# Kernel optimization log

Hardware: AMD Instinct MI355X
Metric: run time of the kernel (lower is better)

## Reference

```python
import jax, jax.numpy as jnp
import numpy as np

EPS = 1e-6
NUM_SPECIAL = 4
NUM_HEADS = 16


def _rms_norm(x, w, eps=EPS):
    # x: [..., d], normalize over last dim
    var = jnp.mean(jnp.square(x), axis=-1, keepdims=True)
    return x * jax.lax.rsqrt(var + eps) * w


def _rotate_half(x):
    d = x.shape[-1] // 2
    return jnp.concatenate([-x[..., d:], x[..., :d]], axis=-1)


def _apply_rotary(q, k, cos, sin):
    # q,k: [B,H,N,hd]; cos,sin: [N,hd] -> broadcast [1,1,N,hd]
    cos = cos[None, None, :, :]
    sin = sin[None, None, :, :]
    q_out = q * cos + _rotate_half(q) * sin
    k_out = k * cos + _rotate_half(k) * sin
    return q_out, k_out


def _make_2d_mask(seq_len, num_special, window):
    # special tokens attend / are attended fully; patches use 2D local box
    patch_len = seq_len - num_special
    gs = int(round(patch_len ** 0.5))
    idx = jnp.arange(seq_len)
    special = idx < num_special
    p = idx - num_special
    row = p // gs
    col = p % gs
    special_case = special[:, None] | special[None, :]
    swa = (jnp.abs(row[:, None] - row[None, :]) <= window) & (
        jnp.abs(col[:, None] - col[None, :]) <= window)
    return special_case | swa  # [N, N] bool


def setup_inputs() -> dict:
    key = jax.random.key(0)
    ks = jax.random.split(key, 7)
    B, N, C = 4, 1028, 1024
    hd = C // NUM_HEADS
    return {
        "hidden_states": jax.random.normal(ks[0], (B, N, C), dtype=jnp.float32),
        "cos": jax.random.uniform(ks[1], (N, hd), dtype=jnp.float32),
        "sin": jax.random.uniform(ks[2], (N, hd), dtype=jnp.float32),
        "qkv_w": jax.random.normal(ks[3], (3 * C, C), dtype=jnp.float32) * (C ** -0.5),
        "out_w": jax.random.normal(ks[4], (C, C), dtype=jnp.float32) * (C ** -0.5),
        "norm_q_w": jnp.ones((hd,), dtype=jnp.float32),
        "norm_k_w": jnp.ones((hd,), dtype=jnp.float32),
        "sliding_window": 2,
    }


def reference(hidden_states, cos, sin, qkv_w, out_w, norm_q_w, norm_k_w, sliding_window):
    B, N, C = hidden_states.shape
    H = NUM_HEADS
    hd = C // H

    # fused QKV projection (nn.Linear: x @ W^T)
    qkv = jnp.einsum('bnc,dc->bnd', hidden_states, qkv_w)
    qkv = qkv.reshape(B, N, 3, H, hd).transpose(2, 0, 3, 1, 4)  # [3,B,H,N,hd]
    q, k, v = qkv[0], qkv[1], qkv[2]

    # per-head-dim RMSNorm on q and k
    q = _rms_norm(q, norm_q_w)
    k = _rms_norm(k, norm_k_w)

    # RoPE
    q, k = _apply_rotary(q, k, cos, sin)

    # 2D sliding-window + special-token mask
    mask = _make_2d_mask(N, NUM_SPECIAL, sliding_window)  # [N,N]

    scale = 1.0 / jnp.sqrt(jnp.asarray(hd, dtype=q.dtype))
    scores = jnp.einsum('bhqd,bhkd->bhqk', q, k) * scale
    neg = jnp.asarray(jnp.finfo(scores.dtype).min, dtype=scores.dtype)
    scores = jnp.where(mask[None, None, :, :], scores, neg)
    probs = jax.nn.softmax(scores, axis=-1)
    attn = jnp.einsum('bhqk,bhkd->bhqd', probs, v)  # [B,H,N,hd]

    attn = attn.transpose(0, 2, 1, 3).reshape(B, N, C)
    return jnp.einsum('bnc,dc->bnd', attn, out_w)
```

## Files before the change

kernel.cpp:

```cpp
#include <hip/hip_runtime.h>
#include <hip/hip_bf16.h>
#include <stdint.h>

typedef __bf16 bf16;
typedef __attribute__((ext_vector_type(8))) __bf16 bf16x8;
typedef __attribute__((ext_vector_type(4))) __bf16 bf16x4;
typedef __attribute__((ext_vector_type(4))) float f32x4;

#define NSEQ 1028
#define CDIM 1024
#define NHEADS 16
#define HD 64
#define BHN 64
#define NPAD 1088
#define M_REAL 4112
#define M_PAD 4224
#define M_PAD256 4352

static __device__ __forceinline__ void async_copy16(bf16* lds, const bf16* g) {
  __builtin_amdgcn_global_load_lds(
      (const __attribute__((address_space(1))) uint32_t*)g,
      (__attribute__((address_space(3))) uint32_t*)lds, 16, 0, 0);
}

__global__ __launch_bounds__(256) void cast_pad_kernel(const float* __restrict__ src,
                                                       bf16* __restrict__ dst,
                                                       long n_src, long n_dst) {
  long t = (long)blockIdx.x * 256 + threadIdx.x;
  long stride = (long)gridDim.x * 256;
  for (long j = t * 4; j < n_dst; j += stride * 4) {
    bf16x4 o;
    if (j + 4 <= n_src) {
      float4 v = *(const float4*)(src + j);
      o[0] = (bf16)v.x; o[1] = (bf16)v.y; o[2] = (bf16)v.z; o[3] = (bf16)v.w;
    } else {
      for (int k = 0; k < 4; k++) o[k] = (bf16)((j + k < n_src) ? src[j + k] : 0.0f);
    }
    *(bf16x4*)(dst + j) = o;
  }
}

__global__ __launch_bounds__(512, 2) void gemm_qkv_256(
    const bf16* __restrict__ A, const bf16* __restrict__ Bm,
    bf16* __restrict__ q_bf, bf16* __restrict__ k_bf, bf16* __restrict__ v_raw,
    const float* __restrict__ cosb, const float* __restrict__ sinb,
    const float* __restrict__ nqw, const float* __restrict__ nkw) {
  constexpr int K = CDIM;
  constexpr int NT = K / 64;
  __shared__ __attribute__((aligned(16))) bf16 As[2 * 2 * 128 * 64];
  __shared__ __attribute__((aligned(16))) bf16 Bs[2 * 2 * 128 * 64];
  const int tid = threadIdx.x;
  const int lane = tid & 63;
  const int wid = tid >> 6;
  const int wr = wid >> 2;
  const int wc = wid & 3;
  const int l15 = lane & 15, l4 = lane >> 4;
  const int rsw = l15 & 7;

  const int nwg = gridDim.x;
  const int qq = nwg >> 3, rr = nwg & 7;
  const int xcd = blockIdx.x & 7, pos = blockIdx.x >> 3;
  const int work = (xcd < rr ? xcd * (qq + 1) : rr * (qq + 1) + (xcd - rr) * qq) + pos;
  const int n0 = (work % 12) << 8;
  const int m0 = (work / 12) << 8;

  f32x4 acc[8][4] = {};
  bf16x8 afr[4][2], bfr0[2][2], bfr1[2][2];

  size_t a_src[2], b_src[2];
#pragma unroll
  for (int s = 0; s < 2; s++) {
    int idx = tid + s * 512;
    int row = idx >> 3, ch = idx & 7, chs = ch ^ (row & 7);
    a_src[s] = (size_t)(m0 + row) * K + (chs << 3);
    b_src[s] = (size_t)(n0 + row) * K + (chs << 3);
  }

#define STAGE_A(bufi, h, tt)                                                   \
  { _Pragma("unroll") for (int s = 0; s < 2; s++)                              \
      async_copy16(&As[((bufi) * 2 + (h)) * 8192 + (tid + s * 512) * 8],       \
                   A + a_src[s] + (size_t)(h) * (128 * K) + (size_t)(tt) * 64); }
#define STAGE_B(bufi, h, tt)                                                   \
  { _Pragma("unroll") for (int s = 0; s < 2; s++)                              \
      async_copy16(&Bs[((bufi) * 2 + (h)) * 8192 + (tid + s * 512) * 8],       \
                   Bm + b_src[s] + (size_t)(h) * (128 * K) + (size_t)(tt) * 64); }
#define LDA_FRAG(mq)                                                           \
  { _Pragma("unroll") for (int ii = 0; ii < 4; ii++)                           \
      _Pragma("unroll") for (int kk = 0; kk < 2; kk++)                         \
        afr[ii][kk] = *(const bf16x8*)&As[abase + (((mq)*4 + ii) * 16 + l15) * 64 + \
                                          (((kk * 4 + l4) ^ rsw) << 3)]; }
#define LDB_FRAG(dst, nq)                                                      \
  { _Pragma("unroll") for (int jj = 0; jj < 2; jj++)                           \
      _Pragma("unroll") for (int kk = 0; kk < 2; kk++)                         \
        dst[jj][kk] = *(const bf16x8*)&Bs[bbase + ((wc & 1) * 64 + ((nq)*2 + jj) * 16 + l15) * 64 + \
                                          (((kk * 4 + l4) ^ rsw) << 3)]; }
#define MFMA_Q(mq, nq, bb)                                                     \
  { _Pragma("unroll") for (int ii = 0; ii < 4; ii++)                           \
      _Pragma("unroll") for (int jj = 0; jj < 2; jj++)                         \
        _Pragma("unroll") for (int kk = 0; kk < 2; kk++)                       \
          acc[(mq)*4 + ii][(nq)*2 + jj] = __builtin_amdgcn_mfma_f32_16x16x32_bf16( \
              afr[ii][kk], bb[jj][kk], acc[(mq)*4 + ii][(nq)*2 + jj], 0, 0, 0); }

  STAGE_A(0, 0, 0); STAGE_A(0, 1, 0); STAGE_B(0, 0, 0); STAGE_B(0, 1, 0);
  STAGE_B(1, 0, 1); STAGE_B(1, 1, 1);
  asm volatile("s_waitcnt vmcnt(4)" ::: "memory");
  __builtin_amdgcn_s_barrier();

  for (int t = 0; t < NT; ++t) {
    const int cur = t & 1, nxt = cur ^ 1;
    const int abase = (cur * 2 + wr) * 8192;
    const int bbase = (cur * 2 + (wc >> 1)) * 8192;
    LDA_FRAG(0); LDB_FRAG(bfr0, 0);
    if (t + 1 < NT) STAGE_A(nxt, 0, t + 1);
    __builtin_amdgcn_s_barrier();
    asm volatile("s_waitcnt lgkmcnt(0)" ::: "memory");
    __builtin_amdgcn_sched_barrier(0);
    __builtin_amdgcn_s_setprio(1);
    MFMA_Q(0, 0, bfr0);
    __builtin_amdgcn_s_setprio(0);
    __builtin_amdgcn_s_barrier();
    LDB_FRAG(bfr1, 1);
    if (t + 1 < NT) STAGE_A(nxt, 1, t + 1);
    __builtin_amdgcn_s_barrier();
    asm volatile("s_waitcnt lgkmcnt(0)" ::: "memory");
    __builtin_amdgcn_sched_barrier(0);
    __builtin_amdgcn_s_setprio(1);
    MFMA_Q(0, 1, bfr1);
    __builtin_amdgcn_s_setprio(0);
    __builtin_amdgcn_s_barrier();
    LDA_FRAG(1);
    if (t + 2 < NT) STAGE_B(cur, 0, t + 2);
    __builtin_amdgcn_s_barrier();
    asm volatile("s_waitcnt lgkmcnt(0)" ::: "memory");
    __builtin_amdgcn_sched_barrier(0);
    __builtin_amdgcn_s_setprio(1);
    MFMA_Q(1, 0, bfr0);
    __builtin_amdgcn_s_setprio(0);
    __builtin_amdgcn_s_barrier();
    if (t + 2 < NT) {
      STAGE_B(cur, 1, t + 2);
      asm volatile("s_waitcnt vmcnt(4)" ::: "memory");
    } else {
      asm volatile("s_waitcnt vmcnt(0)" ::: "memory");
    }
    __builtin_amdgcn_s_barrier();
    __builtin_amdgcn_s_setprio(1);
    MFMA_Q(1, 1, bfr1);
    __builtin_amdgcn_s_setprio(0);
    __builtin_amdgcn_s_barrier();
  }
#undef STAGE_A
#undef STAGE_B
#undef LDA_FRAG
#undef LDB_FRAG
#undef MFMA_Q

  const int d_base = n0 + wc * 64;
  const int tsel = d_base >> 10;
  const int hh = (d_base & 1023) >> 6;
  if (tsel == 2) {
#pragma unroll
    for (int i = 0; i < 8; i++)
#pragma unroll
      for (int r = 0; r < 4; r++) {
        int m = m0 + wr * 128 + i * 16 + l4 * 4 + r;
        if (m < M_REAL) {
          int b = m / NSEQ, n = m % NSEQ;
          size_t rb = ((size_t)(b * NHEADS + hh) * NSEQ + n) * HD;
#pragma unroll
          for (int j = 0; j < 4; j++)
            v_raw[rb + j * 16 + l15] = (bf16)acc[i][j][r];
        }
      }
  } else {
    const float* wn = (tsel == 0) ? nqw : nkw;
    bf16* dst = (tsel == 0) ? q_bf : k_bf;
    float wv[4];
#pragma unroll
    for (int j = 0; j < 4; j++) wv[j] = wn[j * 16 + l15];
#pragma unroll
    for (int i = 0; i < 8; i++)
#pragma unroll
      for (int r = 0; r < 4; r++) {
        int m = m0 + wr * 128 + i * 16 + l4 * 4 + r;
        if (m >= M_REAL) continue;
        float ss = 0.0f;
#pragma unroll
        for (int j = 0; j < 4; j++) { float x = acc[i][j][r]; ss += x * x; }
        ss += __shfl_xor(ss, 1);
        ss += __shfl_xor(ss, 2);
        ss += __shfl_xor(ss, 4);
        ss += __shfl_xor(ss, 8);
        float rms = rsqrtf(ss * (1.0f / HD) + 1e-6f);
        int b = m / NSEQ, n = m % NSEQ;
        float qn[4];
#pragma unroll
        for (int j = 0; j < 4; j++) qn[j] = acc[i][j][r] * rms * wv[j];
        size_t rb = ((size_t)(b * NHEADS + hh) * NPAD + n) * HD;
#pragma unroll
        for (int j = 0; j < 4; j++) {
          float c = cosb[n * HD + j * 16 + l15];
          float s = sinb[n * HD + j * 16 + l15];
          float rot = (j < 2) ? -qn[j + 2] : qn[j - 2];
          dst[rb + j * 16 + l15] = (bf16)(qn[j] * c + rot * s);
        }
      }
  }
}

__global__ __launch_bounds__(256) void gemm_out_kernel(
    const bf16* __restrict__ A, const bf16* __restrict__ Bm, int K, int N, int Mreal,
    float* __restrict__ outF) {
  __shared__ __attribute__((aligned(16))) bf16 As[2][128 * 64];
  __shared__ __attribute__((aligned(16))) bf16 Bs[2][128 * 64];
  const int tid = threadIdx.x;
  const int lane = tid & 63;
  const int wid = tid >> 6;
  const int wr = wid >> 1, wc = wid & 1;
  const int l15 = lane & 15, l4 = lane >> 4;

  const int nwg = gridDim.x;
  const int cpx = nwg >> 3;
  const int work = (blockIdx.x & 7) * cpx + (blockIdx.x >> 3);
  const int ntx = N >> 7;
  const int n0 = (work % ntx) << 7;
  const int m0 = (work / ntx) << 7;

  f32x4 acc[4][4] = {};

  size_t a_base[4], b_base[4];
#pragma unroll
  for (int s = 0; s < 4; s++) {
    int c = tid + s * 256;
    int row = c >> 3, ch = c & 7;
    int chs = ch ^ (row & 7);
    a_base[s] = (size_t)(m0 + row) * K + (chs << 3);
    b_base[s] = (size_t)(n0 + row) * K + (chs << 3);
  }

#define STAGE(bufi, ktof)                                         \
  {                                                               \
    _Pragma("unroll")                                             \
    for (int s = 0; s < 4; s++) {                                 \
      int c = tid + s * 256;                                      \
      async_copy16(&As[bufi][c * 8], A + a_base[s] + (ktof));     \
      async_copy16(&Bs[bufi][c * 8], Bm + b_base[s] + (ktof));    \
    }                                                             \
  }

  const int nt = K >> 6;
  STAGE(0, 0);

  for (int t = 0; t < nt; ++t) {
    if (t + 1 < nt) {
      STAGE((t + 1) & 1, (t + 1) << 6);
      asm volatile("s_waitcnt vmcnt(8)" ::: "memory");
    } else {
      asm volatile("s_waitcnt vmcnt(0)" ::: "memory");
    }
    __builtin_amdgcn_s_barrier();

    const int rsw = l15 & 7;
    const int cur = t & 1;
    bf16x8 af[2][4], bfr[2][4];
#pragma unroll
    for (int h = 0; h < 2; h++)
#pragma unroll
      for (int i = 0; i < 4; i++)
        af[h][i] = *(const bf16x8*)&As[cur][(wr * 64 + i * 16 + l15) * 64 +
                                            (((h * 4 + l4) ^ rsw) << 3)];
#pragma unroll
    for (int h = 0; h < 2; h++)
#pragma unroll
      for (int j = 0; j < 4; j++)
        bfr[h][j] = *(const bf16x8*)&Bs[cur][(wc * 64 + j * 16 + l15) * 64 +
                                             (((h * 4 + l4) ^ rsw) << 3)];

#pragma unroll
    for (int h = 0; h < 2; h++)
#pragma unroll
      for (int i = 0; i < 4; i++)
#pragma unroll
        for (int j = 0; j < 4; j++)
          acc[i][j] = __builtin_amdgcn_mfma_f32_16x16x32_bf16(af[h][i], bfr[h][j], acc[i][j], 0, 0, 0);

    asm volatile("s_waitcnt lgkmcnt(0)" ::: "memory");
    __builtin_amdgcn_s_barrier();
  }
#undef STAGE

#pragma unroll
  for (int i = 0; i < 4; i++)
#pragma unroll
    for (int j = 0; j < 4; j++) {
      int d = n0 + wc * 64 + j * 16 + l15;
      int mrow = m0 + wr * 64 + i * 16 + l4 * 4;
#pragma unroll
      for (int r = 0; r < 4; r++) {
        int m = mrow + r;
        if (m < Mreal) outF[(size_t)m * N + d] = acc[i][j][r];
      }
    }
}

__global__ __launch_bounds__(256) void v_transpose_kernel(const bf16* __restrict__ v_raw,
                                                          bf16* __restrict__ vT) {
  __shared__ bf16 tile[64][65];
  int bh = blockIdx.y, c = blockIdx.x;
  int tid = threadIdx.x;
#pragma unroll
  for (int jj = 0; jj < 16; jj++) {
    int idx = tid + jj * 256;
    int i = idx >> 6, e = idx & 63;
    int n = (c == 0) ? i : (64 * c - 60 + i);
    bool ok = (c == 0) ? (i < 4) : (n < NSEQ);
    tile[i][e] = ok ? v_raw[((size_t)bh * NSEQ + n) * HD + e] : (bf16)0.0f;
  }
  __syncthreads();
#pragma unroll
  for (int jj = 0; jj < 16; jj++) {
    int idx = tid + jj * 256;
    int e = idx >> 6, i = idx & 63;
    vT[((size_t)bh * HD + e) * NPAD + 64 * c + i] = tile[i][e];
  }
}

__global__ __launch_bounds__(256) void attn_kernel(
    const bf16* __restrict__ Q, const bf16* __restrict__ Kb, const bf16* __restrict__ Vt,
    bf16* __restrict__ att, const int* __restrict__ winp) {
  __shared__ __attribute__((aligned(16))) bf16 P_s[4][16][72];
  __shared__ float o_s[4][4][64];
  __shared__ float ml_s[4][2][16];
  const int bh = blockIdx.y, qt = blockIdx.x;
  const int W = winp[0];
  const int tid = threadIdx.x, w = tid >> 6, lane = tid & 63;
  const int l15 = lane & 15, l4 = lane >> 4;
  const size_t qkbase = (size_t)bh * NPAD * HD;
  const size_t vtb = (size_t)bh * HD * NPAD;
  const bool is_spec = (qt == 16);

  const int qrow0 = is_spec ? 0 : (4 + qt * 64 + w * 16);
  bf16x8 aq0 = *(const bf16x8*)&Q[qkbase + (size_t)(qrow0 + l15) * HD + l4 * 8];
  bf16x8 aq1 = *(const bf16x8*)&Q[qkbase + (size_t)(qrow0 + l15) * HD + 32 + l4 * 8];

  float mrow[4], lrow[4];
  f32x4 o[4] = {};
#pragma unroll
  for (int r = 0; r < 4; r++) { mrow[r] = -1e30f; lrow[r] = 0.0f; }

  int p0, pstep, pmax, toff;
  if (is_spec) {
    p0 = w; pstep = 4; pmax = 16; toff = -1;
  } else {
    int ta = ((2 * qt - W + 64) >> 1) - 32;
    int tb = (2 * qt + 1 + W) >> 1;
    ta = ta < 0 ? 0 : ta;
    tb = tb > 15 ? 15 : tb;
    p0 = 0; pstep = 1; pmax = tb - ta + 1; toff = ta - 1;
  }

  for (int p = p0; p <= pmax; p += pstep) {
    const bool sp = (p == 0);
    const int tau = toff + p;
    const int krow0 = sp ? 0 : (4 + tau * 64);
    const int vcol0 = sp ? 0 : (64 + tau * 64);

    f32x4 sacc[4] = {};
#pragma unroll
    for (int kf = 0; kf < 4; kf++) {
      const bf16* kp = &Kb[qkbase + (size_t)(krow0 + kf * 16 + l15) * HD];
      bf16x8 b0 = *(const bf16x8*)(kp + l4 * 8);
      bf16x8 b1 = *(const bf16x8*)(kp + 32 + l4 * 8);
      sacc[kf] = __builtin_amdgcn_mfma_f32_16x16x32_bf16(aq0, b0, sacc[kf], 0, 0, 0);
      sacc[kf] = __builtin_amdgcn_mfma_f32_16x16x32_bf16(aq1, b1, sacc[kf], 0, 0, 0);
    }

    float pvv[4][4];
#pragma unroll
    for (int kf = 0; kf < 4; kf++)
#pragma unroll
      for (int r = 0; r < 4; r++) {
        float s = sacc[kf][r] * 0.125f;
        bool valid;
        if (sp) {
          valid = (kf == 0) && (l15 < 4);
        } else if (is_spec) {
          valid = true;
        } else {
          int p_k = tau * 64 + kf * 16 + l15;
          int p_q = qt * 64 + w * 16 + l4 * 4 + r;
          int dr = (p_q >> 5) - (p_k >> 5); dr = dr < 0 ? -dr : dr;
          int dc = (p_q & 31) - (p_k & 31); dc = dc < 0 ? -dc : dc;
          valid = (dr <= W) && (dc <= W);
        }
        pvv[kf][r] = valid ? s : -1e30f;
      }

#pragma unroll
    for (int r = 0; r < 4; r++) {
      float mx = fmaxf(fmaxf(pvv[0][r], pvv[1][r]), fmaxf(pvv[2][r], pvv[3][r]));
#pragma unroll
      for (int mm = 1; mm < 16; mm <<= 1) mx = fmaxf(mx, __shfl_xor(mx, mm));
      float mnew = fmaxf(mrow[r], mx);
      float scale = __expf(mrow[r] - mnew);
      float rs = 0.0f;
#pragma unroll
      for (int kf = 0; kf < 4; kf++) {
        float pp = __expf(pvv[kf][r] - mnew);
        pvv[kf][r] = pp;
        rs += pp;
      }
#pragma unroll
      for (int mm = 1; mm < 16; mm <<= 1) rs += __shfl_xor(rs, mm);
      lrow[r] = lrow[r] * scale + rs;
      mrow[r] = mnew;
#pragma unroll
      for (int f = 0; f < 4; f++) o[f][r] *= scale;
    }

#pragma unroll
    for (int kf = 0; kf < 4; kf++)
#pragma unroll
      for (int r = 0; r < 4; r++)
        P_s[w][l4 * 4 + r][kf * 16 + l15] = (bf16)pvv[kf][r];

    bf16x8 pa0 = *(const bf16x8*)&P_s[w][l15][l4 * 8];
    bf16x8 pa1 = *(const bf16x8*)&P_s[w][l15][32 + l4 * 8];
#pragma unroll
    for (int f = 0; f < 4; f++) {
      const bf16* vp = &Vt[vtb + (size_t)(f * 16 + l15) * NPAD + vcol0];
      bf16x8 v0 = *(const bf16x8*)(vp + l4 * 8);
      bf16x8 v1 = *(const bf16x8*)(vp + 32 + l4 * 8);
      o[f] = __builtin_amdgcn_mfma_f32_16x16x32_bf16(pa0, v0, o[f], 0, 0, 0);
      o[f] = __builtin_amdgcn_mfma_f32_16x16x32_bf16(pa1, v1, o[f], 0, 0, 0);
    }
  }

  const int b = bh >> 4, h = bh & 15;
  if (!is_spec) {
#pragma unroll
    for (int f = 0; f < 4; f++)
#pragma unroll
      for (int r = 0; r < 4; r++) {
        int n = qrow0 + l4 * 4 + r;
        att[((size_t)(b * NSEQ + n)) * CDIM + h * HD + f * 16 + l15] =
            (bf16)(o[f][r] / lrow[r]);
      }
  } else {
    if (l4 == 0) {
#pragma unroll
      for (int f = 0; f < 4; f++)
#pragma unroll
        for (int r = 0; r < 4; r++) o_s[w][r][f * 16 + l15] = o[f][r];
      if (l15 == 0)
#pragma unroll
        for (int r = 0; r < 4; r++) { ml_s[w][0][r] = mrow[r]; ml_s[w][1][r] = lrow[r]; }
    }
    __syncthreads();
    int row = tid >> 6, dim = tid & 63;
    float M = -1e30f;
#pragma unroll
    for (int ww = 0; ww < 4; ww++) M = fmaxf(M, ml_s[ww][0][row]);
    float L = 0.0f, val = 0.0f;
#pragma unroll
    for (int ww = 0; ww < 4; ww++) {
      float e = __expf(ml_s[ww][0][row] - M);
      L += e * ml_s[ww][1][row];
      val += e * o_s[ww][row][dim];
    }
    att[((size_t)(b * NSEQ + row)) * CDIM + h * HD + dim] = (bf16)(val / L);
  }
}

extern "C" void kernel_launch(void* const* d_in, const int* in_sizes, int n_in,
                              void* d_out, int out_size, void* d_ws, size_t ws_size,
                              hipStream_t stream) {
  const float* hidden = (const float*)d_in[0];
  const float* cosb = (const float*)d_in[1];
  const float* sinb = (const float*)d_in[2];
  const float* qkv_w = (const float*)d_in[3];
  const float* out_w = (const float*)d_in[4];
  const float* norm_q_w = (const float*)d_in[5];
  const float* norm_k_w = (const float*)d_in[6];
  const int* win = (const int*)d_in[7];
  float* out = (float*)d_out;

  char* ws = (char*)d_ws;
  size_t off = 0;
  auto alloc = [&](size_t bytes) {
    char* p = ws + off;
    off += (bytes + 255) & ~(size_t)255;
    return p;
  };
  bf16* A_bf  = (bf16*)alloc((size_t)M_PAD256 * CDIM * 2);
  bf16* W1    = (bf16*)alloc((size_t)3 * CDIM * CDIM * 2);
  bf16* W2    = (bf16*)alloc((size_t)CDIM * CDIM * 2);
  bf16* v_raw = (bf16*)alloc((size_t)BHN * NSEQ * HD * 2);
  bf16* q_bf  = (bf16*)alloc((size_t)BHN * NPAD * HD * 2);
  bf16* k_bf  = (bf16*)alloc((size_t)BHN * NPAD * HD * 2);
  bf16* vT    = (bf16*)alloc((size_t)BHN * HD * NPAD * 2);
  bf16* att   = (bf16*)alloc((size_t)M_PAD * CDIM * 2);
  (void)ws_size; (void)in_sizes; (void)n_in; (void)out_size;

  cast_pad_kernel<<<2048, 256, 0, stream>>>(hidden, A_bf, (long)M_REAL * CDIM, (long)M_PAD256 * CDIM);
  cast_pad_kernel<<<1024, 256, 0, stream>>>(qkv_w, W1, (long)3 * CDIM * CDIM, (long)3 * CDIM * CDIM);
  cast_pad_kernel<<<512, 256, 0, stream>>>(out_w, W2, (long)CDIM * CDIM, (long)CDIM * CDIM);

  gemm_qkv_256<<<204, 512, 0, stream>>>(A_bf, W1, q_bf, k_bf, v_raw,
                                        cosb, sinb, norm_q_w, norm_k_w);
  v_transpose_kernel<<<dim3(17, 64), 256, 0, stream>>>(v_raw, vT);
  attn_kernel<<<dim3(17, 64), 256, 0, stream>>>(q_bf, k_bf, vT, att, win);
  gemm_out_kernel<<<264, 256, 0, stream>>>(att, W2, CDIM, CDIM, M_REAL, out);
}
```

Before: 135.3 us.

## Split-K the output GEMM with atomics, shift the last QKV tile, relax LDS waits

The output projection GEMM is split along K into two halves, doubling the workgroup count to 528, and partial sums are combined with fp32 atomicAdd into an output zeroed by hipMemsetAsync. The QKV GEMM now handles the last M tile by shifting it back to end at the real row count, so the padded 256-row input region and its zero-fill cast are no longer needed. Inside the QKV loop, the lgkmcnt waits and sched_barriers before each MFMA group are removed, and waits are added only before the barriers that precede LDS reuse. These changes aim to improve occupancy and reduce wasted padding work, at the cost of atomic traffic, an extra memset, and non-deterministic summation order.

```diff
diff --git a/kernel.cpp b/kernel.cpp
--- a/kernel.cpp
+++ b/kernel.cpp
@@ -15,7 +15,6 @@
 #define NPAD 1088
 #define M_REAL 4112
 #define M_PAD 4224
-#define M_PAD256 4352
 
 static __device__ __forceinline__ void async_copy16(bf16* lds, const bf16* g) {
   __builtin_amdgcn_global_load_lds(
@@ -62,7 +61,8 @@
   const int xcd = blockIdx.x & 7, pos = blockIdx.x >> 3;
   const int work = (xcd < rr ? xcd * (qq + 1) : rr * (qq + 1) + (xcd - rr) * qq) + pos;
   const int n0 = (work % 12) << 8;
-  const int m0 = (work / 12) << 8;
+  const int mi = work / 12;
+  const int m0 = (mi < 16) ? (mi << 8) : (M_REAL - 256);
 
   f32x4 acc[8][4] = {};
   bf16x8 afr[4][2], bfr0[2][2], bfr1[2][2];
@@ -113,8 +113,6 @@
     LDA_FRAG(0); LDB_FRAG(bfr0, 0);
     if (t + 1 < NT) STAGE_A(nxt, 0, t + 1);
     __builtin_amdgcn_s_barrier();
-    asm volatile("s_waitcnt lgkmcnt(0)" ::: "memory");
-    __builtin_amdgcn_sched_barrier(0);
     __builtin_amdgcn_s_setprio(1);
     MFMA_Q(0, 0, bfr0);
     __builtin_amdgcn_s_setprio(0);
@@ -122,17 +120,14 @@
     LDB_FRAG(bfr1, 1);
     if (t + 1 < NT) STAGE_A(nxt, 1, t + 1);
     __builtin_amdgcn_s_barrier();
-    asm volatile("s_waitcnt lgkmcnt(0)" ::: "memory");
-    __builtin_amdgcn_sched_barrier(0);
     __builtin_amdgcn_s_setprio(1);
     MFMA_Q(0, 1, bfr1);
     __builtin_amdgcn_s_setprio(0);
+    asm volatile("s_waitcnt lgkmcnt(0)" ::: "memory");
     __builtin_amdgcn_s_barrier();
     LDA_FRAG(1);
     if (t + 2 < NT) STAGE_B(cur, 0, t + 2);
     __builtin_amdgcn_s_barrier();
-    asm volatile("s_waitcnt lgkmcnt(0)" ::: "memory");
-    __builtin_amdgcn_sched_barrier(0);
     __builtin_amdgcn_s_setprio(1);
     MFMA_Q(1, 0, bfr0);
     __builtin_amdgcn_s_setprio(0);
@@ -147,6 +142,7 @@
     __builtin_amdgcn_s_setprio(1);
     MFMA_Q(1, 1, bfr1);
     __builtin_amdgcn_s_setprio(0);
+    asm volatile("s_waitcnt lgkmcnt(0)" ::: "memory");
     __builtin_amdgcn_s_barrier();
   }
 #undef STAGE_A
@@ -209,8 +205,11 @@
 }
 
 __global__ __launch_bounds__(256) void gemm_out_kernel(
-    const bf16* __restrict__ A, const bf16* __restrict__ Bm, int K, int N, int Mreal,
+    const bf16* __restrict__ A, const bf16* __restrict__ Bm,
     float* __restrict__ outF) {
+  constexpr int LDK = CDIM;
+  constexpr int KH = 512;
+  constexpr int N = CDIM;
   __shared__ __attribute__((aligned(16))) bf16 As[2][128 * 64];
   __shared__ __attribute__((aligned(16))) bf16 Bs[2][128 * 64];
   const int tid = threadIdx.x;
@@ -222,9 +221,11 @@
   const int nwg = gridDim.x;
   const int cpx = nwg >> 3;
   const int work = (blockIdx.x & 7) * cpx + (blockIdx.x >> 3);
-  const int ntx = N >> 7;
-  const int n0 = (work % ntx) << 7;
-  const int m0 = (work / ntx) << 7;
+  const int ks = work / 264;
+  const int rem = work % 264;
+  const int n0 = (rem & 7) << 7;
+  const int m0 = (rem >> 3) << 7;
+  const size_t kbase = (size_t)ks * KH;
 
   f32x4 acc[4][4] = {};
 
@@ -234,8 +235,8 @@
     int c = tid + s * 256;
     int row = c >> 3, ch = c & 7;
     int chs = ch ^ (row & 7);
-    a_base[s] = (size_t)(m0 + row) * K + (chs << 3);
-    b_base[s] = (size_t)(n0 + row) * K + (chs << 3);
+    a_base[s] = (size_t)(m0 + row) * LDK + kbase + (chs << 3);
+    b_base[s] = (size_t)(n0 + row) * LDK + kbase + (chs << 3);
   }
 
 #define STAGE(bufi, ktof)                                         \
@@ -248,7 +249,7 @@
     }                                                             \
   }
 
-  const int nt = K >> 6;
+  const int nt = KH >> 6;
   STAGE(0, 0);
 
   for (int t = 0; t < nt; ++t) {
@@ -298,7 +299,7 @@
 #pragma unroll
       for (int r = 0; r < 4; r++) {
         int m = mrow + r;
-        if (m < Mreal) outF[(size_t)m * N + d] = acc[i][j][r];
+        if (m < M_REAL) atomicAdd(&outF[(size_t)m * N + d], acc[i][j][r]);
       }
     }
 }
@@ -492,7 +493,7 @@
     off += (bytes + 255) & ~(size_t)255;
     return p;
   };
-  bf16* A_bf  = (bf16*)alloc((size_t)M_PAD256 * CDIM * 2);
+  bf16* A_bf  = (bf16*)alloc((size_t)M_REAL * CDIM * 2);
   bf16* W1    = (bf16*)alloc((size_t)3 * CDIM * CDIM * 2);
   bf16* W2    = (bf16*)alloc((size_t)CDIM * CDIM * 2);
   bf16* v_raw = (bf16*)alloc((size_t)BHN * NSEQ * HD * 2);
@@ -502,7 +503,9 @@
   bf16* att   = (bf16*)alloc((size_t)M_PAD * CDIM * 2);
   (void)ws_size; (void)in_sizes; (void)n_in; (void)out_size;
 
-  cast_pad_kernel<<<2048, 256, 0, stream>>>(hidden, A_bf, (long)M_REAL * CDIM, (long)M_PAD256 * CDIM);
+  hipMemsetAsync(out, 0, (size_t)M_REAL * CDIM * sizeof(float), stream);
+
+  cast_pad_kernel<<<2048, 256, 0, stream>>>(hidden, A_bf, (long)M_REAL * CDIM, (long)M_REAL * CDIM);
   cast_pad_kernel<<<1024, 256, 0, stream>>>(qkv_w, W1, (long)3 * CDIM * CDIM, (long)3 * CDIM * CDIM);
   cast_pad_kernel<<<512, 256, 0, stream>>>(out_w, W2, (long)CDIM * CDIM, (long)CDIM * CDIM);
 
@@ -510,5 +513,5 @@
                                         cosb, sinb, norm_q_w, norm_k_w);
   v_transpose_kernel<<<dim3(17, 64), 256, 0, stream>>>(v_raw, vT);
   attn_kernel<<<dim3(17, 64), 256, 0, stream>>>(q_bf, k_bf, vT, att, win);
-  gemm_out_kernel<<<264, 256, 0, stream>>>(att, W2, CDIM, CDIM, M_REAL, out);
-}
+  gemm_out_kernel<<<528, 256, 0, stream>>>(att, W2, out);
+}
```

Result: slower. 158.5 us (+17.1%).
